# Optimization experiments

Measured on AMD Instinct MI355X. Metric: run time of the kernel, lower is better.

## Reference

```python
import jax, jax.numpy as jnp
import numpy as np

B, D, H = 8192, 1024, 1024


def _linear_init(key, shape, fan_in):
    bound = 1.0 / np.sqrt(fan_in)
    return jax.random.uniform(key, shape, jnp.float32, -bound, bound)


def setup_inputs() -> dict:
    key = jax.random.key(0)
    ks = jax.random.split(key, 20)
    inp = {
        "x": jax.random.normal(ks[0], (B, D), jnp.float32),
        "h_prev": jax.random.normal(ks[1], (B, H), jnp.float32),
        "c_prev": jax.random.normal(ks[2], (B, H), jnp.float32),
        "C_prev": jax.random.normal(ks[3], (B, H), jnp.float32),
        "n_prev": jax.random.uniform(ks[4], (B, H), jnp.float32),
        "m_prev": jax.random.normal(ks[5], (B, H), jnp.float32),
    }
    # input projections Wz/Wi/Wf/Wo: Linear(D -> H) with bias
    for i, g in enumerate("ziofo"[:4]):
        pass
    names = ["z", "i", "f", "o"]
    for j, g in enumerate(names):
        inp[f"W{g}"] = _linear_init(ks[6 + j], (H, D), D)
        inp[f"b{g}"] = _linear_init(ks[10 + j], (H,), D)
        inp[f"R{g}"] = _linear_init(ks[14 + j], (H, H), H)  # no bias
    return inp


def reference(x, h_prev, c_prev, C_prev, n_prev, m_prev,
              Wz, bz, Wi, bi, Wf, bf, Wo, bo,
              Rz, Ri, Rf, Ro):
    # Batch the 4 input projections and 4 recurrent projections into 2 GEMMs.
    Wcat = jnp.concatenate([Wi, Wf, Wo, Wz], axis=0)        # [4H, D]
    bcat = jnp.concatenate([bi, bf, bo, bz], axis=0)        # [4H]
    Rcat = jnp.concatenate([Ri, Rf, Ro, Rz], axis=0)        # [4H, H]
    pre = x @ Wcat.T + bcat + h_prev @ Rcat.T               # [B, 4H]
    pi, pf, po, pz = jnp.split(pre, 4, axis=1)

    i = jnp.exp(pi)
    f = jax.nn.sigmoid(pf)
    o = jax.nn.sigmoid(po)
    z = jnp.tanh(pz)

    c = f * c_prev + i * z
    n = f * n_prev + i
    m = jnp.maximum(jnp.log(f) + m_prev, pi)  # log(exp(pi)) == pi
    h = o * (c / n)
    return (h, c, C_prev, n, m)
```

## Files before the change

### kernel.cpp

```cpp
#include <hip/hip_runtime.h>


#define B_SZ 8192
#define D_SZ 1024
#define H_SZ 1024
#define K_SZ 2048
#define N4H  4096

typedef __attribute__((ext_vector_type(4))) float f32x4;
typedef _Float16 f16;
typedef __attribute__((ext_vector_type(8))) f16 f16x8;
typedef unsigned short u16;
typedef __attribute__((ext_vector_type(4))) unsigned short u16x4;

static __device__ __forceinline__ u16 f2h(float f) {
    f16 h = (f16)f;
    return __builtin_bit_cast(unsigned short, h);
}

static __device__ __forceinline__ void load_lds16(const void* g, void* l) {
    __builtin_amdgcn_global_load_lds(
        (const __attribute__((address_space(1))) void*)g,
        (__attribute__((address_space(3))) void*)l, 16, 0, 0);
}

__global__ void convert_A(const float* __restrict__ x, const float* __restrict__ h,
                          u16* __restrict__ A) {
    const size_t nvec = (size_t)B_SZ * K_SZ / 4;
    const size_t stride = (size_t)gridDim.x * blockDim.x;
    for (size_t v = (size_t)blockIdx.x * blockDim.x + threadIdx.x; v < nvec; v += stride) {
        size_t e = v * 4;
        size_t row = e >> 11;
        int col = (int)(e & 2047);
        const float* src = (col < D_SZ) ? (x + row * D_SZ + col)
                                        : (h + row * H_SZ + (col - D_SZ));
        f32x4 val = *(const f32x4*)src;
        u16x4 o;
        o[0] = f2h(val[0]); o[1] = f2h(val[1]); o[2] = f2h(val[2]); o[3] = f2h(val[3]);
        *(u16x4*)(A + e) = o;
    }
}

__global__ void convert_W(const float* __restrict__ Wi, const float* __restrict__ Wf,
                          const float* __restrict__ Wo, const float* __restrict__ Wz,
                          const float* __restrict__ Ri, const float* __restrict__ Rf,
                          const float* __restrict__ Ro, const float* __restrict__ Rz,
                          u16* __restrict__ Wb) {
    const size_t nvec = (size_t)N4H * K_SZ / 4;
    const size_t stride = (size_t)gridDim.x * blockDim.x;
    for (size_t v = (size_t)blockIdx.x * blockDim.x + threadIdx.x; v < nvec; v += stride) {
        size_t e = v * 4;
        size_t r = e >> 11;
        int col = (int)(e & 2047);
        int g = (int)(r >> 4) & 3;
        int j = (int)((r >> 6) << 4) | (int)(r & 15);
        const float* Wg = (g == 0) ? Wi : (g == 1) ? Wf : (g == 2) ? Wo : Wz;
        const float* Rg = (g == 0) ? Ri : (g == 1) ? Rf : (g == 2) ? Ro : Rz;
        const float* src = (col < D_SZ) ? (Wg + (size_t)j * D_SZ + col)
                                        : (Rg + (size_t)j * H_SZ + (col - D_SZ));
        f32x4 val = *(const f32x4*)src;
        u16x4 o;
        o[0] = f2h(val[0]); o[1] = f2h(val[1]); o[2] = f2h(val[2]); o[3] = f2h(val[3]);
        *(u16x4*)(Wb + e) = o;
    }
}

__global__ __launch_bounds__(256, 2)
void gemm_fused(const u16* __restrict__ A, const u16* __restrict__ W,
                const float* __restrict__ c_prev, const float* __restrict__ n_prev,
                const float* __restrict__ m_prev,
                const float* __restrict__ bi, const float* __restrict__ bfv,
                const float* __restrict__ bo, const float* __restrict__ bz,
                float* __restrict__ out) {
    __shared__ u16 lA[128 * 64];
    __shared__ u16 lB[128 * 64];

    const int tid = threadIdx.x;
    const int w  = tid >> 6;
    const int l  = tid & 63;
    const int wm = w >> 1;
    const int wn = w & 1;
    const int m0 = blockIdx.x * 128;
    const int n0 = blockIdx.y * 128;

    const int lrow8 = l >> 3;
    const int lseg  = (l & 7) ^ lrow8;

    const int fr = l & 15;
    const int kq = l >> 4;

    f32x4 acc[4][4] = {};

    for (int kt = 0; kt < K_SZ; kt += 64) {
#pragma unroll
        for (int r = 0; r < 4; ++r) {
            int rowA = r * 32 + w * 8 + lrow8;
            const u16* gA = A + (size_t)(m0 + rowA) * K_SZ + kt + lseg * 8;
            load_lds16(gA, (char*)lA + (r * 32 + w * 8) * 128);
            const u16* gB = W + (size_t)(n0 + rowA) * K_SZ + kt + lseg * 8;
            load_lds16(gB, (char*)lB + (r * 32 + w * 8) * 128);
        }
        __syncthreads();

#pragma unroll
        for (int ks = 0; ks < 2; ++ks) {
            f16x8 af[4], bfr[4];
#pragma unroll
            for (int mi = 0; mi < 4; ++mi) {
                int row = wm * 64 + mi * 16 + fr;
                int seg = (ks * 4 + kq) ^ (row & 7);
                af[mi] = *(const f16x8*)&lA[row * 64 + seg * 8];
            }
#pragma unroll
            for (int ni = 0; ni < 4; ++ni) {
                int row = wn * 64 + ni * 16 + fr;
                int seg = (ks * 4 + kq) ^ (row & 7);
                bfr[ni] = *(const f16x8*)&lB[row * 64 + seg * 8];
            }
#pragma unroll
            for (int mi = 0; mi < 4; ++mi)
#pragma unroll
                for (int ni = 0; ni < 4; ++ni)
                    acc[mi][ni] = __builtin_amdgcn_mfma_f32_16x16x32_f16(
                        af[mi], bfr[ni], acc[mi][ni], 0, 0, 0);
        }
        __syncthreads();
    }

    const size_t BH = (size_t)B_SZ * H_SZ;
    const int j = ((n0 + wn * 64) >> 6) * 16 + fr;
    const float bvi = bi[j], bvf = bfv[j], bvo = bo[j], bvz = bz[j];

#pragma unroll
    for (int mi = 0; mi < 4; ++mi) {
        const int rbase = m0 + wm * 64 + mi * 16 + kq * 4;
#pragma unroll
        for (int r2 = 0; r2 < 4; ++r2) {
            const size_t idx = (size_t)(rbase + r2) * H_SZ + j;
            float pi = acc[mi][0][r2] + bvi;
            float pf = acc[mi][1][r2] + bvf;
            float po = acc[mi][2][r2] + bvo;
            float pz = acc[mi][3][r2] + bvz;
            float iv = __expf(pi);
            float fv = 1.0f / (1.0f + __expf(-pf));
            float ov = 1.0f / (1.0f + __expf(-po));
            float e2 = __expf(2.0f * pz);
            float zv = 1.0f - 2.0f / (e2 + 1.0f);
            float cv = fv * c_prev[idx] + iv * zv;
            float nv = fv * n_prev[idx] + iv;
            float mv = fmaxf(__logf(fv) + m_prev[idx], pi);
            out[idx]          = ov * (cv / nv);
            out[BH + idx]     = cv;
            out[3 * BH + idx] = nv;
            out[4 * BH + idx] = mv;
        }
    }
}

extern "C" void kernel_launch(void* const* d_in, const int* in_sizes, int n_in,
                              void* d_out, int out_size, void* d_ws, size_t ws_size,
                              hipStream_t stream) {
    const float* x      = (const float*)d_in[0];
    const float* h_prev = (const float*)d_in[1];
    const float* c_prev = (const float*)d_in[2];
    const float* C_prev = (const float*)d_in[3];
    const float* n_prev = (const float*)d_in[4];
    const float* m_prev = (const float*)d_in[5];
    const float* Wz = (const float*)d_in[6];
    const float* bz = (const float*)d_in[7];
    const float* Rz = (const float*)d_in[8];
    const float* Wi = (const float*)d_in[9];
    const float* bi = (const float*)d_in[10];
    const float* Ri = (const float*)d_in[11];
    const float* Wf = (const float*)d_in[12];
    const float* bf = (const float*)d_in[13];
    const float* Rf = (const float*)d_in[14];
    const float* Wo = (const float*)d_in[15];
    const float* bo = (const float*)d_in[16];
    const float* Ro = (const float*)d_in[17];
    float* out = (float*)d_out;

    const size_t BH = (size_t)B_SZ * H_SZ;

    u16* Abuf = (u16*)d_ws;
    u16* Wbuf = (u16*)((char*)d_ws + (size_t)32 * 1024 * 1024);

    convert_A<<<2048, 256, 0, stream>>>(x, h_prev, Abuf);
    convert_W<<<2048, 256, 0, stream>>>(Wi, Wf, Wo, Wz, Ri, Rf, Ro, Rz, Wbuf);

    hipMemcpyAsync(out + 2 * BH, C_prev, BH * sizeof(float),
                   hipMemcpyDeviceToDevice, stream);

    gemm_fused<<<dim3(B_SZ / 128, N4H / 128), 256, 0, stream>>>(
        Abuf, Wbuf, c_prev, n_prev, m_prev, bi, bf, bo, bz, out);
}
```

Before: 225.8 us.

## Merge convert kernels, fold C_prev copy into GEMM epilogue, prioritize MFMA

Merges the two fp16 conversion kernels into one launch, removes the separate device-to-device memcpy of C_prev by copying it inside the GEMM epilogue, and raises wave priority around the MFMA block. The epilogue now batches the c/C/n/m loads for each row group ahead of the math. The aim is fewer launches and less duplicated memory traffic. In exchange the epilogue does an extra strided load and store per element, and register pressure rises.

New measurement: 218.7 us. 1.03x faster.

```diff
diff --git a/kernel.cpp b/kernel.cpp
--- a/kernel.cpp
+++ b/kernel.cpp
@@ -24,51 +24,49 @@
         (__attribute__((address_space(3))) void*)l, 16, 0, 0);
 }
 
-__global__ void convert_A(const float* __restrict__ x, const float* __restrict__ h,
-                          u16* __restrict__ A) {
-    const size_t nvec = (size_t)B_SZ * K_SZ / 4;
+__global__ void convert_AW(const float* __restrict__ x, const float* __restrict__ h,
+                           const float* __restrict__ Wi, const float* __restrict__ Wf,
+                           const float* __restrict__ Wo, const float* __restrict__ Wz,
+                           const float* __restrict__ Ri, const float* __restrict__ Rf,
+                           const float* __restrict__ Ro, const float* __restrict__ Rz,
+                           u16* __restrict__ A, u16* __restrict__ Wb) {
+    const size_t nvecA = (size_t)B_SZ * K_SZ / 4;
+    const size_t nvecW = (size_t)N4H * K_SZ / 4;
+    const size_t nvec  = nvecA + nvecW;
     const size_t stride = (size_t)gridDim.x * blockDim.x;
     for (size_t v = (size_t)blockIdx.x * blockDim.x + threadIdx.x; v < nvec; v += stride) {
-        size_t e = v * 4;
-        size_t row = e >> 11;
-        int col = (int)(e & 2047);
-        const float* src = (col < D_SZ) ? (x + row * D_SZ + col)
-                                        : (h + row * H_SZ + (col - D_SZ));
+        const float* src;
+        u16* dst;
+        if (v < nvecA) {
+            size_t e = v * 4;
+            size_t row = e >> 11;
+            int col = (int)(e & 2047);
+            src = (col < D_SZ) ? (x + row * D_SZ + col)
+                               : (h + row * H_SZ + (col - D_SZ));
+            dst = A + e;
+        } else {
+            size_t e = (v - nvecA) * 4;
+            size_t r = e >> 11;
+            int col = (int)(e & 2047);
+            int g = (int)(r >> 4) & 3;
+            int j = (int)((r >> 6) << 4) | (int)(r & 15);
+            const float* Wg = (g == 0) ? Wi : (g == 1) ? Wf : (g == 2) ? Wo : Wz;
+            const float* Rg = (g == 0) ? Ri : (g == 1) ? Rf : (g == 2) ? Ro : Rz;
+            src = (col < D_SZ) ? (Wg + (size_t)j * D_SZ + col)
+                               : (Rg + (size_t)j * H_SZ + (col - D_SZ));
+            dst = Wb + e;
+        }
         f32x4 val = *(const f32x4*)src;
         u16x4 o;
         o[0] = f2h(val[0]); o[1] = f2h(val[1]); o[2] = f2h(val[2]); o[3] = f2h(val[3]);
-        *(u16x4*)(A + e) = o;
-    }
-}
-
-__global__ void convert_W(const float* __restrict__ Wi, const float* __restrict__ Wf,
-                          const float* __restrict__ Wo, const float* __restrict__ Wz,
-                          const float* __restrict__ Ri, const float* __restrict__ Rf,
-                          const float* __restrict__ Ro, const float* __restrict__ Rz,
-                          u16* __restrict__ Wb) {
-    const size_t nvec = (size_t)N4H * K_SZ / 4;
-    const size_t stride = (size_t)gridDim.x * blockDim.x;
-    for (size_t v = (size_t)blockIdx.x * blockDim.x + threadIdx.x; v < nvec; v += stride) {
-        size_t e = v * 4;
-        size_t r = e >> 11;
-        int col = (int)(e & 2047);
-        int g = (int)(r >> 4) & 3;
-        int j = (int)((r >> 6) << 4) | (int)(r & 15);
-        const float* Wg = (g == 0) ? Wi : (g == 1) ? Wf : (g == 2) ? Wo : Wz;
-        const float* Rg = (g == 0) ? Ri : (g == 1) ? Rf : (g == 2) ? Ro : Rz;
-        const float* src = (col < D_SZ) ? (Wg + (size_t)j * D_SZ + col)
-                                        : (Rg + (size_t)j * H_SZ + (col - D_SZ));
-        f32x4 val = *(const f32x4*)src;
-        u16x4 o;
-        o[0] = f2h(val[0]); o[1] = f2h(val[1]); o[2] = f2h(val[2]); o[3] = f2h(val[3]);
-        *(u16x4*)(Wb + e) = o;
+        *(u16x4*)dst = o;
     }
 }
 
 __global__ __launch_bounds__(256, 2)
 void gemm_fused(const u16* __restrict__ A, const u16* __restrict__ W,
-                const float* __restrict__ c_prev, const float* __restrict__ n_prev,
-                const float* __restrict__ m_prev,
+                const float* __restrict__ c_prev, const float* __restrict__ C_prev,
+                const float* __restrict__ n_prev, const float* __restrict__ m_prev,
                 const float* __restrict__ bi, const float* __restrict__ bfv,
                 const float* __restrict__ bo, const float* __restrict__ bz,
                 float* __restrict__ out) {
@@ -117,12 +115,14 @@
                 int seg = (ks * 4 + kq) ^ (row & 7);
                 bfr[ni] = *(const f16x8*)&lB[row * 64 + seg * 8];
             }
+            __builtin_amdgcn_s_setprio(1);
 #pragma unroll
             for (int mi = 0; mi < 4; ++mi)
 #pragma unroll
                 for (int ni = 0; ni < 4; ++ni)
                     acc[mi][ni] = __builtin_amdgcn_mfma_f32_16x16x32_f16(
                         af[mi], bfr[ni], acc[mi][ni], 0, 0, 0);
+            __builtin_amdgcn_s_setprio(0);
         }
         __syncthreads();
     }
@@ -134,6 +134,15 @@
 #pragma unroll
     for (int mi = 0; mi < 4; ++mi) {
         const int rbase = m0 + wm * 64 + mi * 16 + kq * 4;
+        float cp[4], Cp[4], np[4], mp[4];
+#pragma unroll
+        for (int r2 = 0; r2 < 4; ++r2) {
+            const size_t idx = (size_t)(rbase + r2) * H_SZ + j;
+            cp[r2] = c_prev[idx];
+            Cp[r2] = C_prev[idx];
+            np[r2] = n_prev[idx];
+            mp[r2] = m_prev[idx];
+        }
 #pragma unroll
         for (int r2 = 0; r2 < 4; ++r2) {
             const size_t idx = (size_t)(rbase + r2) * H_SZ + j;
@@ -146,11 +155,12 @@
             float ov = 1.0f / (1.0f + __expf(-po));
             float e2 = __expf(2.0f * pz);
             float zv = 1.0f - 2.0f / (e2 + 1.0f);
-            float cv = fv * c_prev[idx] + iv * zv;
-            float nv = fv * n_prev[idx] + iv;
-            float mv = fmaxf(__logf(fv) + m_prev[idx], pi);
+            float cv = fv * cp[r2] + iv * zv;
+            float nv = fv * np[r2] + iv;
+            float mv = fmaxf(__logf(fv) + mp[r2], pi);
             out[idx]          = ov * (cv / nv);
             out[BH + idx]     = cv;
+            out[2 * BH + idx] = Cp[r2];
             out[3 * BH + idx] = nv;
             out[4 * BH + idx] = mv;
         }
@@ -180,17 +190,12 @@
     const float* Ro = (const float*)d_in[17];
     float* out = (float*)d_out;
 
-    const size_t BH = (size_t)B_SZ * H_SZ;
-
     u16* Abuf = (u16*)d_ws;
     u16* Wbuf = (u16*)((char*)d_ws + (size_t)32 * 1024 * 1024);
 
-    convert_A<<<2048, 256, 0, stream>>>(x, h_prev, Abuf);
-    convert_W<<<2048, 256, 0, stream>>>(Wi, Wf, Wo, Wz, Ri, Rf, Ro, Rz, Wbuf);
-
-    hipMemcpyAsync(out + 2 * BH, C_prev, BH * sizeof(float),
-                   hipMemcpyDeviceToDevice, stream);
+    convert_AW<<<2048, 256, 0, stream>>>(x, h_prev, Wi, Wf, Wo, Wz,
+                                         Ri, Rf, Ro, Rz, Abuf, Wbuf);
 
     gemm_fused<<<dim3(B_SZ / 128, N4H / 128), 256, 0, stream>>>(
-        Abuf, Wbuf, c_prev, n_prev, m_prev, bi, bf, bo, bz, out);
-}
+        Abuf, Wbuf, c_prev, C_prev, n_prev, m_prev, bi, bf, bo, bz, out);
+}
```
